# Optimization experiments

Hardware: AMD Instinct MI355X
Metric: run time of the kernel (lower is better)

## Reference

```python
import jax, jax.numpy as jnp
import numpy as np

S, D = 4096, 2048  # seq_len, embedding_space == qkv_dim


def setup_inputs() -> dict:
    key = jax.random.key(0)
    k1, k2, k3, k4, k5 = jax.random.split(key, 5)
    return {
        "input_embedding": jax.random.normal(k1, (S, D), dtype=jnp.float32),
        "query_embedding": jax.random.normal(k2, (S, D), dtype=jnp.float32),
        "Wq": jax.random.normal(k3, (D, D), dtype=jnp.float32) * 0.02,
        "Wk": jax.random.normal(k4, (D, D), dtype=jnp.float32) * 0.02,
        "Wv": jax.random.normal(k5, (D, D), dtype=jnp.float32) * 0.02,
        "include_mask": 0,  # False -> causal mask applied (module's inverted logic)
    }


def reference(input_embedding, query_embedding, Wq, Wk, Wv, include_mask):
    q = query_embedding @ Wq          # [S, D]
    k = input_embedding @ Wk          # [S, D]
    v = input_embedding @ Wv          # [S, D]
    scores = (q @ k.T) / 10.0         # [S, S]; module hardcodes /10, not sqrt(d)
    if not include_mask:
        # causal: -inf strictly above the diagonal (triu with offset 1)
        s = scores.shape[0]
        causal = jnp.tril(jnp.ones((s, s), dtype=bool))
        scores = jnp.where(causal, scores, -jnp.inf)
    probs = jax.nn.softmax(scores, axis=-1)
    return probs @ v                  # [S, D]
```

## Files before the change

kernel.cpp:

```cpp
#include <hip/hip_runtime.h>
#include <hip/hip_bf16.h>
#include <math.h>

typedef __bf16 bf16_t;
typedef __bf16 bf16x8 __attribute__((ext_vector_type(8)));
typedef float f32x4 __attribute__((ext_vector_type(4)));

enum { EP_BF16 = 0, EP_SCORES = 1, EP_F32 = 2, EP_F32A = 3 };

#define MEMFENCE asm volatile("" ::: "memory")
#define BARRIER() do { MEMFENCE; __builtin_amdgcn_s_barrier(); MEMFENCE; } while (0)

__device__ __forceinline__ void gload_lds16(const void* g, void* l) {
  __builtin_amdgcn_global_load_lds(
      (const __attribute__((address_space(1))) void*)g,
      (__attribute__((address_space(3))) void*)l, 16, 0, 0);
}

__device__ __forceinline__ int xcd_swz(int bid, int nwg) {
  const int q = nwg >> 3;
  return (bid & 7) * q + (bid >> 3);
}


template <int TM, bool STG>
__device__ __forceinline__ void do_tile(char* smem, int slot, int sslot, size_t stoff,
                                        const char* const* gbase, const int* lbase,
                                        const int* aoff, const int* boff,
                                        f32x4 (&acc)[TM][4]) {
  bf16x8 bfr[4], af[4];
  if constexpr (TM == 8) {
#pragma unroll
    for (int n = 0; n < 4; ++n) bfr[n] = *(const bf16x8*)(smem + slot + boff[n]);
#pragma unroll
    for (int m = 0; m < 4; ++m) af[m] = *(const bf16x8*)(smem + slot + aoff[m]);
    if constexpr (STG) {
      gload_lds16(gbase[0] + stoff, smem + sslot + lbase[0]);
      gload_lds16(gbase[1] + stoff, smem + sslot + lbase[1]);
    }
    BARRIER();
    asm volatile("s_waitcnt lgkmcnt(0)" ::: "memory");
    __builtin_amdgcn_sched_barrier(0);
    __builtin_amdgcn_s_setprio(1);
#pragma unroll
    for (int m = 0; m < 4; ++m)
#pragma unroll
      for (int n = 0; n < 4; ++n)
        acc[m][n] = __builtin_amdgcn_mfma_f32_16x16x32_bf16(af[m], bfr[n], acc[m][n], 0, 0, 0);
    __builtin_amdgcn_s_setprio(0);
    BARRIER();
#pragma unroll
    for (int m = 0; m < 4; ++m) af[m] = *(const bf16x8*)(smem + slot + aoff[4 + m]);
    if constexpr (STG) {
      gload_lds16(gbase[2] + stoff, smem + sslot + lbase[2]);
      gload_lds16(gbase[3] + stoff, smem + sslot + lbase[3]);
      asm volatile("s_waitcnt vmcnt(8)" ::: "memory");
    }
    BARRIER();
    asm volatile("s_waitcnt lgkmcnt(0)" ::: "memory");
    __builtin_amdgcn_sched_barrier(0);
    __builtin_amdgcn_s_setprio(1);
#pragma unroll
    for (int m = 0; m < 4; ++m)
#pragma unroll
      for (int n = 0; n < 4; ++n)
        acc[4 + m][n] = __builtin_amdgcn_mfma_f32_16x16x32_bf16(af[m], bfr[n], acc[4 + m][n], 0, 0, 0);
    __builtin_amdgcn_s_setprio(0);
    BARRIER();
  } else {
#pragma unroll
    for (int n = 0; n < 4; ++n) bfr[n] = *(const bf16x8*)(smem + slot + boff[n]);
#pragma unroll
    for (int m = 0; m < 4; ++m) af[m] = *(const bf16x8*)(smem + slot + aoff[m]);
    if constexpr (STG) {
      gload_lds16(gbase[0] + stoff, smem + sslot + lbase[0]);
      gload_lds16(gbase[1] + stoff, smem + sslot + lbase[1]);
      gload_lds16(gbase[2] + stoff, smem + sslot + lbase[2]);
      asm volatile("s_waitcnt vmcnt(6)" ::: "memory");
    }
    BARRIER();
    asm volatile("s_waitcnt lgkmcnt(0)" ::: "memory");
    __builtin_amdgcn_sched_barrier(0);
    __builtin_amdgcn_s_setprio(1);
#pragma unroll
    for (int m = 0; m < 4; ++m)
#pragma unroll
      for (int n = 0; n < 4; ++n)
        acc[m][n] = __builtin_amdgcn_mfma_f32_16x16x32_bf16(af[m], bfr[n], acc[m][n], 0, 0, 0);
    __builtin_amdgcn_s_setprio(0);
    BARRIER();
  }
}

template <int TM, int EPI>
__device__ __forceinline__ void gemm_core(
    const bf16_t* __restrict__ A, const bf16_t* __restrict__ B,
    void* __restrict__ Cout, int Nout, int kstride, int klen,
    int row0, int col0, bool causal, float scale, char* smem)
{
  constexpr int BM = TM * 32;
  constexpr int LPT_A = BM / 128;
  constexpr int LPT = LPT_A + 2;
  constexpr int ABYTES = BM * 64;
  constexpr int SLOT = (BM + 256) * 64;

  const int tid = threadIdx.x;
  const int w = tid >> 6, lane = tid & 63;
  const int wr = w >> 2, wc = w & 3;

  const int nt = klen >> 5;

  const char* gbase[LPT];
  int lbase[LPT];
  {
    const int sd = (tid & 3) ^ ((tid >> 3) & 3);
    const int rrow = tid >> 2;
#pragma unroll
    for (int r = 0; r < LPT; ++r) {
      const bool isA = (r < LPT_A);
      const int rr = isA ? r : (r - LPT_A);
      const int grow = (isA ? row0 : col0) + rr * 128 + rrow;
      const bf16_t* op = isA ? A : B;
      gbase[r] = (const char*)(op + (size_t)grow * kstride) + sd * 16;
      lbase[r] = (isA ? 0 : ABYTES) + rr * 8192 + w * 1024;
    }
  }

  const int fl = lane & 15;
  const int arow_off = fl * 64 + (((lane >> 4) ^ ((fl >> 1) & 3)) * 16);
  int aoff[TM], boff[4];
#pragma unroll
  for (int m = 0; m < TM; ++m) aoff[m] = (wr * (TM * 16) + m * 16) * 64 + arow_off;
#pragma unroll
  for (int n = 0; n < 4; ++n) boff[n] = ABYTES + (wc * 64 + n * 16) * 64 + arow_off;

  f32x4 acc[TM][4] = {};

  const int npro = nt < 3 ? nt : 3;
  for (int t = 0; t < npro; ++t)
#pragma unroll
    for (int r = 0; r < LPT; ++r)
      gload_lds16(gbase[r] + (size_t)t * 64, smem + (t & 3) * SLOT + lbase[r]);

  const int nmain = nt - 3;
  if (nmain > 0) {
    if constexpr (TM == 8) asm volatile("s_waitcnt vmcnt(8)" ::: "memory");
    else                   asm volatile("s_waitcnt vmcnt(6)" ::: "memory");
    BARRIER();
    for (int t = 0; t < nmain; ++t)
      do_tile<TM, true>(smem, (t & 3) * SLOT, ((t + 3) & 3) * SLOT,
                        (size_t)(t + 3) * 64, gbase, lbase, aoff, boff, acc);
  }

  asm volatile("s_waitcnt vmcnt(0)" ::: "memory");
  BARRIER();
  for (int t = nmain > 0 ? nmain : 0; t < nt; ++t)
    do_tile<TM, false>(smem, (t & 3) * SLOT, 0, 0, gbase, lbase, aoff, boff, acc);

  const int cr = (lane >> 4) * 4;
  const int cc = lane & 15;
#pragma unroll
  for (int m = 0; m < TM; ++m) {
#pragma unroll
    for (int n = 0; n < 4; ++n) {
#pragma unroll
      for (int i = 0; i < 4; ++i) {
        const int r = row0 + wr * (TM * 16) + m * 16 + cr + i;
        const int c = col0 + wc * 64 + n * 16 + cc;
        float v = acc[m][n][i];
        if (EPI == EP_BF16) {
          ((bf16_t*)Cout)[(size_t)r * Nout + c] = (bf16_t)v;
        } else if (EPI == EP_SCORES) {
          v *= scale;
          if (causal && c > r) v = -INFINITY;
          ((float*)Cout)[(size_t)r * Nout + c] = v;
        } else if (EPI == EP_F32) {
          ((float*)Cout)[(size_t)r * Nout + c] = v;
        } else {
          atomicAdd((float*)Cout + (size_t)r * Nout + c, v);
        }
      }
    }
  }
}

__launch_bounds__(512, 2)
__global__ void qk_k(const bf16_t* __restrict__ qe16, const bf16_t* __restrict__ ie16,
                     const bf16_t* __restrict__ WqT, const bf16_t* __restrict__ WkT,
                     bf16_t* __restrict__ q16, bf16_t* __restrict__ k16) {
  extern __shared__ __align__(16) char smem[];
  int wg = xcd_swz(blockIdx.x, gridDim.x);
  const bf16_t *A, *B; bf16_t* C;
  if (wg < 128) { A = qe16; B = WqT; C = q16; }
  else          { A = ie16; B = WkT; C = k16; wg -= 128; }
  const int row0 = (wg >> 3) * 256, col0 = (wg & 7) * 256;
  gemm_core<8, EP_BF16>(A, B, C, 2048, 2048, 2048, row0, col0, false, 1.f, smem);
}

__launch_bounds__(512, 2)
__global__ void vs_k(const bf16_t* __restrict__ WvT, const bf16_t* __restrict__ ie16,
                     const bf16_t* __restrict__ q16, const bf16_t* __restrict__ k16,
                     bf16_t* __restrict__ vT16, float* __restrict__ scores,
                     const int* __restrict__ maskflag) {
  extern __shared__ __align__(16) char smem[];
  const bool causal = maskflag[0] == 0;
  const int nsc = causal ? 136 : 256;
  const int bid = blockIdx.x;
  if (bid < nsc) {
    const int sid = xcd_swz(bid, nsc);
    int r, c;
    if (causal) {
      r = (int)((sqrtf(8.f * (float)sid + 1.f) - 1.f) * 0.5f);
      while ((r + 1) * (r + 2) / 2 <= sid) ++r;
      while (r * (r + 1) / 2 > sid) --r;
      c = sid - r * (r + 1) / 2;
    } else {
      r = sid >> 4; c = sid & 15;
    }
    gemm_core<8, EP_SCORES>(q16, k16, scores, 4096, 2048, 2048,
                            r * 256, c * 256, causal, 0.1f, smem);
  } else {
    const int j = bid - nsc;
    gemm_core<4, EP_BF16>(WvT, ie16, vT16, 4096, 2048, 2048,
                          (j >> 4) * 128, (j & 15) * 256, false, 1.f, smem);
  }
}

__launch_bounds__(512, 2)
__global__ void smv_k(const bf16_t* __restrict__ WvT, const bf16_t* __restrict__ ie16,
                      bf16_t* __restrict__ vT16,
                      const float* __restrict__ scores, bf16_t* __restrict__ probs,
                      const int* __restrict__ maskflag) {
  extern __shared__ __align__(16) char smem[];
  const bool causal = maskflag[0] == 0;
  const int nv = causal ? 136 : 256;
  const int vbase = causal ? 120 : 0;
  const int bid = blockIdx.x;
  if (bid < nv) {
    const int j = vbase + bid;
    gemm_core<4, EP_BF16>(WvT, ie16, vT16, 4096, 2048, 2048,
                          (j >> 4) * 128, (j & 15) * 256, false, 1.f, smem);
    return;
  }
  const int p = bid - nv;
  if (p >= 2048) return;
  const int tid = threadIdx.x;
  const int h = tid >> 8;
  const int t = tid & 255;
  const int row = 2 * p + h;
  const int L = causal ? (row + 1) : 4096;
  const float* srow = scores + (size_t)row * 4096;
  float v[16];
  float m = -INFINITY;
#pragma unroll
  for (int j = 0; j < 16; ++j) {
    const int idx = t + j * 256;
    v[j] = (idx < L) ? srow[idx] : -INFINITY;
    m = fmaxf(m, v[j]);
  }
#pragma unroll
  for (int off = 32; off >= 1; off >>= 1) m = fmaxf(m, __shfl_xor(m, off));
  __shared__ float redm[8];
  __shared__ float reds[8];
  if ((tid & 63) == 0) redm[tid >> 6] = m;
  __syncthreads();
  m = fmaxf(fmaxf(redm[4 * h + 0], redm[4 * h + 1]),
            fmaxf(redm[4 * h + 2], redm[4 * h + 3]));
  float s = 0.f;
#pragma unroll
  for (int j = 0; j < 16; ++j) {
    v[j] = __expf(v[j] - m);
    s += v[j];
  }
#pragma unroll
  for (int off = 32; off >= 1; off >>= 1) s += __shfl_xor(s, off);
  if ((tid & 63) == 0) reds[tid >> 6] = s;
  __syncthreads();
  s = reds[4 * h + 0] + reds[4 * h + 1] + reds[4 * h + 2] + reds[4 * h + 3];
  const float inv = 1.f / s;
  bf16_t* prow = probs + (size_t)row * 4096;
#pragma unroll
  for (int j = 0; j < 16; ++j) prow[t + j * 256] = (bf16_t)(v[j] * inv);
}

__launch_bounds__(512, 2)
__global__ void pv_k(const bf16_t* __restrict__ probs, const bf16_t* __restrict__ vT16,
                     float* __restrict__ out, const int* __restrict__ maskflag) {
  extern __shared__ __align__(16) char smem[];
  const bool causal = maskflag[0] == 0;
  const int bid = blockIdx.x;
  int band, col, k0, klen; bool at;
  if (causal) {
    if (bid < 256) {
      const int t = bid >> 1;
      band = 16 + (t >> 3); col = t & 7;
      const int Keff = 128 * (band + 1);
      klen = Keff >> 1; k0 = (bid & 1) ? klen : 0; at = true;
    } else if (bid < 384) {
      const int t = bid - 256;
      band = t >> 3; col = t & 7;
      k0 = 0; klen = 128 * (band + 1); at = false;
    } else return;
  } else {
    if (bid >= 512) return;
    const int t = bid >> 1;
    band = t >> 3; col = t & 7;
    klen = 2048; k0 = (bid & 1) ? 2048 : 0; at = true;
  }
  if (at)
    gemm_core<4, EP_F32A>(probs + k0, vT16 + k0, out, 2048, 4096, klen,
                          band * 128, col * 256, false, 1.f, smem);
  else
    gemm_core<4, EP_F32>(probs + k0, vT16 + k0, out, 2048, 4096, klen,
                         band * 128, col * 256, false, 1.f, smem);
}


__global__ void cvt_k(const float* __restrict__ qe, const float* __restrict__ ie,
                      bf16_t* __restrict__ qe16, bf16_t* __restrict__ ie16,
                      float* __restrict__ zout, long n) {
  const int y = blockIdx.y;
  long i = ((long)blockIdx.x * blockDim.x + threadIdx.x) * 8;
  const long stride = (long)gridDim.x * blockDim.x * 8;
  if (y == 2) {
    const float4 z = make_float4(0.f, 0.f, 0.f, 0.f);
    for (; i < n; i += stride) {
      *(float4*)(zout + i) = z;
      *(float4*)(zout + i + 4) = z;
    }
    return;
  }
  const float* x = y ? ie : qe;
  bf16_t* o = y ? ie16 : qe16;
  for (; i < n; i += stride) {
    const float4 a = *(const float4*)(x + i);
    const float4 b = *(const float4*)(x + i + 4);
    bf16x8 u;
    u[0] = (__bf16)a.x; u[1] = (__bf16)a.y; u[2] = (__bf16)a.z; u[3] = (__bf16)a.w;
    u[4] = (__bf16)b.x; u[5] = (__bf16)b.y; u[6] = (__bf16)b.z; u[7] = (__bf16)b.w;
    *(bf16x8*)(o + i) = u;
  }
}

__global__ void trans_k(const float* __restrict__ Wq, const float* __restrict__ Wk,
                        const float* __restrict__ Wv,
                        bf16_t* __restrict__ WqT, bf16_t* __restrict__ WkT,
                        bf16_t* __restrict__ WvT, int Dm) {
  const float* W = blockIdx.z == 0 ? Wq : (blockIdx.z == 1 ? Wk : Wv);
  bf16_t* WT = blockIdx.z == 0 ? WqT : (blockIdx.z == 1 ? WkT : WvT);
  __shared__ float tile[32][33];
  const int bx = blockIdx.x, by = blockIdx.y;
  const int tx = threadIdx.x & 31, ty = threadIdx.x >> 5;
#pragma unroll
  for (int r = ty; r < 32; r += 8)
    tile[r][tx] = W[(size_t)(by * 32 + r) * Dm + bx * 32 + tx];
  __syncthreads();
#pragma unroll
  for (int r = ty; r < 32; r += 8)
    WT[(size_t)(bx * 32 + r) * Dm + by * 32 + tx] = (bf16_t)tile[tx][r];
}

extern "C" void kernel_launch(void* const* d_in, const int* in_sizes, int n_in,
                              void* d_out, int out_size, void* d_ws, size_t ws_size,
                              hipStream_t stream) {
  const float* ie = (const float*)d_in[0];
  const float* qe = (const float*)d_in[1];
  const float* Wq = (const float*)d_in[2];
  const float* Wk = (const float*)d_in[3];
  const float* Wv = (const float*)d_in[4];
  const int* mask = (const int*)d_in[5];
  float* out = (float*)d_out;

  const int S = 4096, D = 2048;
  char* ws = (char*)d_ws;
  const size_t MB = 1u << 20;
  bf16_t* q16  = (bf16_t*)(ws + 0 * MB);
  bf16_t* k16  = (bf16_t*)(ws + 16 * MB);
  bf16_t* vT16 = (bf16_t*)(ws + 32 * MB);
  bf16_t* ie16 = (bf16_t*)(ws + 48 * MB);
  bf16_t* WvT  = (bf16_t*)(ws + 64 * MB);
  bf16_t* qe16 = (bf16_t*)(ws + 72 * MB);
  bf16_t* WqT  = (bf16_t*)(ws + 88 * MB);
  bf16_t* WkT  = (bf16_t*)(ws + 96 * MB);
  float*  scores = (float*)(ws + 72 * MB);
  bf16_t* probs  = (bf16_t*)(ws + 0 * MB);

  hipFuncSetAttribute(reinterpret_cast<const void*>(&qk_k),
                      hipFuncAttributeMaxDynamicSharedMemorySize, 131072);
  hipFuncSetAttribute(reinterpret_cast<const void*>(&vs_k),
                      hipFuncAttributeMaxDynamicSharedMemorySize, 131072);
  hipFuncSetAttribute(reinterpret_cast<const void*>(&smv_k),
                      hipFuncAttributeMaxDynamicSharedMemorySize, 98304);
  hipFuncSetAttribute(reinterpret_cast<const void*>(&pv_k),
                      hipFuncAttributeMaxDynamicSharedMemorySize, 98304);

  cvt_k<<<dim3(1024, 3), 256, 0, stream>>>(qe, ie, qe16, ie16, out, (long)S * D);
  trans_k<<<dim3(D / 32, D / 32, 3), 256, 0, stream>>>(Wq, Wk, Wv, WqT, WkT, WvT, D);

  qk_k<<<256, 512, 131072, stream>>>(qe16, ie16, WqT, WkT, q16, k16);

  vs_k<<<256, 512, 131072, stream>>>(WvT, ie16, q16, k16, vT16, scores, mask);

  smv_k<<<2304, 512, 98304, stream>>>(WvT, ie16, vT16, scores, probs, mask);

  pv_k<<<512, 512, 98304, stream>>>(probs, vT16, out, mask);
}
```

Measured before the change: 282.5 us.

## Balance causal PV work by pairing short and long row bands per block

The causal PV kernel now pairs row band p with band 31-p, so each of 256 blocks handles an equal K length (2112). One block runs the short band fully, then the first part of the long band with atomic accumulation. Its partner runs the remainder of the long band. This replaces the previous uneven 384-block split. Block IDs are also XCD-swizzled so blocks sharing a column land on the same XCD for L2 reuse. The trade-off is more atomic accumulation and a second sequential GEMM inside some blocks.

```diff
diff --git a/kernel.cpp b/kernel.cpp
--- a/kernel.cpp
+++ b/kernel.cpp
@@ -289,30 +289,34 @@
   extern __shared__ __align__(16) char smem[];
   const bool causal = maskflag[0] == 0;
   const int bid = blockIdx.x;
-  int band, col, k0, klen; bool at;
   if (causal) {
-    if (bid < 256) {
-      const int t = bid >> 1;
-      band = 16 + (t >> 3); col = t & 7;
-      const int Keff = 128 * (band + 1);
-      klen = Keff >> 1; k0 = (bid & 1) ? klen : 0; at = true;
-    } else if (bid < 384) {
-      const int t = bid - 256;
-      band = t >> 3; col = t & 7;
-      k0 = 0; klen = 128 * (band + 1); at = false;
-    } else return;
+    if (bid >= 256) return;
+    const int sid  = xcd_swz(bid, 256);
+    const int half = sid & 1;
+    const int pair = (sid >> 1) & 15;
+    const int col  = sid >> 5;
+    const int blo = pair, bhi = 31 - pair;
+    const int Klo = 128 * (blo + 1);
+    const int cut = 2112 - Klo;
+    if (half == 0) {
+      gemm_core<4, EP_F32>(probs, vT16, out, 2048, 4096, Klo,
+                           blo * 128, col * 256, false, 1.f, smem);
+      __syncthreads();
+      gemm_core<4, EP_F32A>(probs, vT16, out, 2048, 4096, cut,
+                            bhi * 128, col * 256, false, 1.f, smem);
+    } else {
+      gemm_core<4, EP_F32A>(probs + cut, vT16 + cut, out, 2048, 4096, 2112,
+                            bhi * 128, col * 256, false, 1.f, smem);
+    }
   } else {
     if (bid >= 512) return;
-    const int t = bid >> 1;
-    band = t >> 3; col = t & 7;
-    klen = 2048; k0 = (bid & 1) ? 2048 : 0; at = true;
-  }
-  if (at)
-    gemm_core<4, EP_F32A>(probs + k0, vT16 + k0, out, 2048, 4096, klen,
+    const int sid = xcd_swz(bid, 512);
+    const int t = sid >> 1;
+    const int band = t & 31, col = t >> 5;
+    const int k0 = (sid & 1) ? 2048 : 0;
+    gemm_core<4, EP_F32A>(probs + k0, vT16 + k0, out, 2048, 4096, 2048,
                           band * 128, col * 256, false, 1.f, smem);
-  else
-    gemm_core<4, EP_F32>(probs + k0, vT16 + k0, out, 2048, 4096, klen,
-                         band * 128, col * 256, false, 1.f, smem);
+  }
 }
 
 
```

New measurement: 275.3 us. -2.5%, faster.
